# Optimization experiments

Hardware: AMD Instinct MI355X
Metric: run time of the kernel (lower is better)

Reference implementation:

```python
import jax, jax.numpy as jnp
import numpy as np

H = 2048  # hidden_size
B, S = 4, 4096
LEVELS = 3  # hierarchical_compression_levels


def _linear_params(key, out_dim, in_dim):
    kw, kb = jax.random.split(key)
    bound = 1.0 / np.sqrt(in_dim)
    W = jax.random.uniform(kw, (out_dim, in_dim), minval=-bound, maxval=bound, dtype=jnp.float32)
    b = jax.random.uniform(kb, (out_dim,), minval=-bound, maxval=bound, dtype=jnp.float32)
    return W, b


def setup_inputs() -> dict:
    key = jax.random.key(0)
    ks = jax.random.split(key, 12)
    inp = {}
    inp['hidden_states'] = jax.random.normal(ks[0], (B, S, H), dtype=jnp.float32)
    inp['access_frequency'] = jax.random.uniform(ks[1], (B, S), dtype=jnp.float32)
    inp['importance_score'] = jax.random.uniform(ks[2], (B, S), dtype=jnp.float32)
    # compression level 1: H -> H/2 -> H/2 -> H ; level 2: H -> H/4 -> H/4 -> H
    inp['comp1_W'], inp['comp1_b'] = _linear_params(ks[3], H // 2, H)
    inp['adapt1_W'], inp['adapt1_b'] = _linear_params(ks[4], H // 2, H // 2)
    inp['decomp1_W'], inp['decomp1_b'] = _linear_params(ks[5], H, H // 2)
    inp['comp2_W'], inp['comp2_b'] = _linear_params(ks[6], H // 4, H)
    inp['adapt2_W'], inp['adapt2_b'] = _linear_params(ks[7], H // 4, H // 4)
    inp['decomp2_W'], inp['decomp2_b'] = _linear_params(ks[8], H, H // 4)
    # strategy selector: Linear(H, H/4) -> ReLU -> Linear(H/4, LEVELS) -> Softmax
    inp['sel1_W'], inp['sel1_b'] = _linear_params(ks[9], H // 4, H)
    inp['sel2_W'], inp['sel2_b'] = _linear_params(ks[10], LEVELS, H // 4)
    return inp


def reference(hidden_states, access_frequency, importance_score,
              comp1_W, comp1_b, adapt1_W, adapt1_b, decomp1_W, decomp1_b,
              comp2_W, comp2_b, adapt2_W, adapt2_b, decomp2_W, decomp2_b,
              sel1_W, sel1_b, sel2_W, sel2_b):
    h = hidden_states
    h2 = h.shape[-1] // 2
    # _get_compression_strategy: scale first half by freq, second half by importance
    combined = jnp.concatenate(
        [h[..., :h2] * access_frequency[..., None],
         h[..., h2:] * importance_score[..., None]], axis=-1)  # [B,S,H]
    hid = jax.nn.relu(jnp.einsum('bsh,oh->bso', combined, sel1_W) + sel1_b)
    strategy_weights = jax.nn.softmax(jnp.einsum('bso,lo->bsl', hid, sel2_W) + sel2_b, axis=-1)
    selected = jnp.argmax(strategy_weights, axis=-1)  # [B,S] int

    def branch(Wc, bc, Wa, ba, Wd, bd):
        c = jnp.einsum('bsh,oh->bso', h, Wc) + bc          # compress
        c = jnp.einsum('bso,po->bsp', c, Wa) + ba          # frequency adaptor
        return jnp.einsum('bsp,hp->bsh', c, Wd) + bd       # decompress

    out1 = branch(comp1_W, comp1_b, adapt1_W, adapt1_b, decomp1_W, decomp1_b)
    out2 = branch(comp2_W, comp2_b, adapt2_W, adapt2_b, decomp2_W, decomp2_b)
    stacked = jnp.stack([h, out1, out2], axis=2)  # [B,S,LEVELS,H]
    compressed = jnp.take_along_axis(stacked, selected[:, :, None, None], axis=2)[:, :, 0, :]
    return compressed
```

## Files before the change

kernel.cpp:

```cpp
#include <hip/hip_runtime.h>
#include <hip/hip_bf16.h>

#define TOK 16384
#define TAU2 0.001f

typedef __attribute__((ext_vector_type(8))) short short8;
typedef __attribute__((ext_vector_type(4))) float f32x4;

__device__ __forceinline__ unsigned short f32_bf16(float f) {
  __hip_bfloat16 h = __float2bfloat16(f);
  unsigned short u;
  __builtin_memcpy(&u, &h, sizeof(u));
  return u;
}
__device__ __forceinline__ float bf16_f32(unsigned short u) {
  union { unsigned int i; float f; } c; c.i = ((unsigned int)u) << 16; return c.f;
}

__device__ __forceinline__ void gll16(const unsigned short* g, unsigned short* l) {
  __builtin_amdgcn_global_load_lds(
      (const __attribute__((address_space(1))) unsigned int*)g,
      (__attribute__((address_space(3))) unsigned int*)l, 16, 0, 0);
}

__global__ void zero3(int* a, int* c) {
  if (threadIdx.x == 0) { *a = 0; c[0] = 0; c[1] = 0; }
}

__global__ void cvt_kernel(const float* __restrict__ s, unsigned short* __restrict__ d, int n4) {
  int i = blockIdx.x * 256 + threadIdx.x;
  if (i < n4) {
    float4 v = ((const float4*)s)[i];
    union { unsigned short u[4]; uint2 q; } pk;
    pk.u[0] = f32_bf16(v.x); pk.u[1] = f32_bf16(v.y);
    pk.u[2] = f32_bf16(v.z); pk.u[3] = f32_bf16(v.w);
    ((uint2*)d)[i] = pk.q;
  }
}

__global__ void cvt_split_kernel(const float* __restrict__ s,
                                 unsigned short* __restrict__ dhi,
                                 unsigned short* __restrict__ dlo, int n4) {
  int i = blockIdx.x * 256 + threadIdx.x;
  if (i < n4) {
    float4 v = ((const float4*)s)[i];
    const float* f = (const float*)&v;
    union { unsigned short u[4]; uint2 q; } hi, lo;
    #pragma unroll
    for (int e = 0; e < 4; e++) {
      unsigned short h = f32_bf16(f[e]);
      hi.u[e] = h;
      lo.u[e] = f32_bf16(f[e] - bf16_f32(h));
    }
    ((uint2*)dhi)[i] = hi.q;
    ((uint2*)dlo)[i] = lo.q;
  }
}

__global__ void compact_sel(const int* __restrict__ sel, int* __restrict__ idx1,
                            int* __restrict__ idx2, int* __restrict__ cnt) {
  int t = blockIdx.x * 256 + threadIdx.x;
  int s = sel[t];
  if (s == 1) idx1[atomicAdd(&cnt[0], 1)] = t;
  else if (s == 2) idx2[atomicAdd(&cnt[1], 1)] = t;
}

__global__ void pad_idx(int* __restrict__ idx1, int* __restrict__ idx2,
                        const int* __restrict__ cnt, int* __restrict__ mc) {
  const int tid = threadIdx.x;
  const int n1 = cnt[0], n2 = cnt[1];
  const int p1 = (n1 + 127) & ~(int)127, p2 = (n2 + 127) & ~(int)127;
  if (tid < p1 - n1) idx1[n1 + tid] = -1;
  if (tid < p2 - n2) idx2[n2 + tid] = -1;
  if (tid == 0) { mc[0] = p1; mc[1] = p2; }
}

template<int EPI, int AG>
__device__ __forceinline__
void gemm_body(const unsigned short* __restrict__ A,
               const unsigned short* __restrict__ Bw,
               const float* __restrict__ bias,
               void* __restrict__ Outv,
               const int* __restrict__ idx, const int* __restrict__ mcp,
               int N, int K) {
  __shared__ __align__(16) unsigned short As[2][128 * 32];
  __shared__ __align__(16) unsigned short Bs[2][128 * 32];
  const int tid = threadIdx.x;
  const int m0 = blockIdx.y * 128, n0 = blockIdx.x * 128;
  if (mcp && m0 >= *mcp) return;
  const int lane = tid & 63, wave = tid >> 6;
  const int wm = wave >> 1, wn = wave & 1;
  const int quad = lane >> 4, lr = lane & 15;

  const int srow = tid >> 2;
  const int schunk = (tid & 3) ^ (srow & 3);
  unsigned int aoff[2], boff[2];
  #pragma unroll
  for (int r = 0; r < 2; r++) {
    int row = r * 64 + srow;
    int gr = m0 + row;
    if (AG) { int t = idx[gr]; gr = (t < 0) ? 0 : t; }
    aoff[r] = (unsigned int)gr * (unsigned int)K + (unsigned int)(schunk * 8);
    boff[r] = (unsigned int)(n0 + row) * (unsigned int)K + (unsigned int)(schunk * 8);
  }
  const int lds_dst = tid * 8;

  f32x4 acc[4][4] = {};
  const int nk = K >> 5;

  #pragma unroll
  for (int r = 0; r < 2; r++) {
    gll16(A + aoff[r], &As[0][r * 2048 + lds_dst]);
    gll16(Bw + boff[r], &Bs[0][r * 2048 + lds_dst]);
  }
  __syncthreads();

  int cur = 0;
  for (int t = 0; t < nk; t++) {
    if (t + 1 < nk) {
      const unsigned int k0 = (unsigned int)(t + 1) << 5;
      #pragma unroll
      for (int r = 0; r < 2; r++) {
        gll16(A + aoff[r] + k0, &As[cur ^ 1][r * 2048 + lds_dst]);
        gll16(Bw + boff[r] + k0, &Bs[cur ^ 1][r * 2048 + lds_dst]);
      }
    }
    short8 af[4], bfr[4];
    #pragma unroll
    for (int i = 0; i < 4; i++) {
      const int row = wm * 64 + i * 16 + lr;
      af[i] = *(const short8*)(&As[cur][row * 32 + ((quad ^ (row & 3)) << 3)]);
    }
    #pragma unroll
    for (int j = 0; j < 4; j++) {
      const int row = wn * 64 + j * 16 + lr;
      bfr[j] = *(const short8*)(&Bs[cur][row * 32 + ((quad ^ (row & 3)) << 3)]);
    }
    #pragma unroll
    for (int i = 0; i < 4; i++)
      #pragma unroll
      for (int j = 0; j < 4; j++)
        acc[i][j] = __builtin_amdgcn_mfma_f32_16x16x32_bf16(af[i], bfr[j], acc[i][j], 0, 0, 0);
    __syncthreads();
    cur ^= 1;
  }

  #pragma unroll
  for (int i = 0; i < 4; i++) {
    const int rbase = m0 + wm * 64 + i * 16 + quad * 4;
    #pragma unroll
    for (int j = 0; j < 4; j++) {
      const int col = n0 + wn * 64 + j * 16 + lr;
      const float bv = bias[col];
      #pragma unroll
      for (int r = 0; r < 4; r++) {
        const int row = rbase + r;
        float v = acc[i][j][r] + bv;
        if (EPI == 0) {
          ((unsigned short*)Outv)[(size_t)row * N + col] = f32_bf16(v);
        } else {
          const int tk = idx[row];
          if (tk >= 0) ((float*)Outv)[(size_t)tk * N + col] = v;
        }
      }
    }
  }
}

#define GEMM_SHELL(NAME, EPI, AG)                                              \
__global__ __launch_bounds__(256, 3) void NAME(                                \
    const unsigned short* __restrict__ A,                                      \
    const unsigned short* __restrict__ Bw,                                     \
    const float* __restrict__ bias, void* __restrict__ Outv,                   \
    const int* __restrict__ idx, const int* __restrict__ mcp, int N, int K) {  \
  gemm_body<EPI, AG>(A, Bw, bias, Outv, idx, mcp, N, K);                       \
}
GEMM_SHELL(g_comp1, 0, 1)
GEMM_SHELL(g_comp2, 0, 1)
GEMM_SHELL(g_adapt1, 0, 0)
GEMM_SHELL(g_adapt2, 0, 0)
GEMM_SHELL(g_dec1, 4, 0)
GEMM_SHELL(g_dec2, 4, 0)

__global__ __launch_bounds__(256, 2)
void gemm_sel(const float* __restrict__ Af,
              const unsigned short* __restrict__ Bw,
              const unsigned short* __restrict__ Bw2,
              const float* __restrict__ bias,
              float* __restrict__ Out,
              const float* __restrict__ scA, const float* __restrict__ scB,
              int N, int K) {
  __shared__ __align__(16) unsigned short As[2 * 128 * 32];
  __shared__ __align__(16) unsigned short Bs[2 * 128 * 32];
  const int LO = 128 * 32;
  const int tid = threadIdx.x;
  const int m0 = blockIdx.y * 128, n0 = blockIdx.x * 128;
  const int lane = tid & 63, wave = tid >> 6;
  const int wm = wave >> 1, wn = wave & 1;
  const int quad = lane >> 4, lr = lane & 15;
  const int srow = tid >> 1, scol = (tid & 1) * 16;

  const size_t aRowOff = (size_t)(m0 + srow) * K;
  const unsigned short* Brow = Bw + (size_t)(n0 + srow) * K;
  const unsigned short* Brow2 = Bw2 + (size_t)(n0 + srow) * K;

  f32x4 acc[4][4] = {};

  for (int k0 = 0; k0 < K; k0 += 32) {
    {
      const float4* src = (const float4*)(Af + aRowOff + k0 + scol);
      float4 f[4];
      f[0] = src[0]; f[1] = src[1]; f[2] = src[2]; f[3] = src[3];
      const int tk = m0 + srow;
      const float s = ((k0 + scol) * 2 < K) ? scA[tk] : scB[tk];
      union { unsigned short u[16]; uint4 q[2]; } hi;
      union { unsigned short u[16]; uint4 q[2]; } lo;
      const float* ff = (const float*)f;
      #pragma unroll
      for (int e = 0; e < 16; e++) {
        float fv = ff[e] * s;
        unsigned short hb = f32_bf16(fv);
        hi.u[e] = hb;
        lo.u[e] = f32_bf16(fv - bf16_f32(hb));
      }
      uint4* dst = (uint4*)(As + srow * 32 + scol);
      dst[0] = hi.q[0]; dst[1] = hi.q[1];
      uint4* dst2 = (uint4*)(As + LO + srow * 32 + scol);
      dst2[0] = lo.q[0]; dst2[1] = lo.q[1];
    }
    {
      const uint4* src = (const uint4*)(Brow + k0 + scol);
      uint4* dst = (uint4*)(Bs + srow * 32 + scol);
      dst[0] = src[0]; dst[1] = src[1];
      const uint4* src2 = (const uint4*)(Brow2 + k0 + scol);
      uint4* dst2 = (uint4*)(Bs + LO + srow * 32 + scol);
      dst2[0] = src2[0]; dst2[1] = src2[1];
    }
    __syncthreads();
    short8 af[4], bfr[4], af2[4], bf2[4];
    #pragma unroll
    for (int i = 0; i < 4; i++) {
      af[i]  = *(const short8*)(As + (wm * 64 + i * 16 + lr) * 32 + quad * 8);
      af2[i] = *(const short8*)(As + LO + (wm * 64 + i * 16 + lr) * 32 + quad * 8);
    }
    #pragma unroll
    for (int j = 0; j < 4; j++) {
      bfr[j] = *(const short8*)(Bs + (wn * 64 + j * 16 + lr) * 32 + quad * 8);
      bf2[j] = *(const short8*)(Bs + LO + (wn * 64 + j * 16 + lr) * 32 + quad * 8);
    }
    #pragma unroll
    for (int i = 0; i < 4; i++)
      #pragma unroll
      for (int j = 0; j < 4; j++) {
        acc[i][j] = __builtin_amdgcn_mfma_f32_16x16x32_bf16(af[i], bfr[j], acc[i][j], 0, 0, 0);
        acc[i][j] = __builtin_amdgcn_mfma_f32_16x16x32_bf16(af[i], bf2[j], acc[i][j], 0, 0, 0);
        acc[i][j] = __builtin_amdgcn_mfma_f32_16x16x32_bf16(af2[i], bfr[j], acc[i][j], 0, 0, 0);
      }
    __syncthreads();
  }

  #pragma unroll
  for (int i = 0; i < 4; i++) {
    const int rbase = m0 + wm * 64 + i * 16 + quad * 4;
    #pragma unroll
    for (int j = 0; j < 4; j++) {
      const int col = n0 + wn * 64 + j * 16 + lr;
      const float bv = bias[col];
      #pragma unroll
      for (int r = 0; r < 4; r++) {
        const int row = rbase + r;
        float v = acc[i][j][r] + bv;
        Out[(size_t)row * N + col] = fmaxf(v, 0.0f);
      }
    }
  }
}

__global__ __launch_bounds__(256)
void selector_logits_f32(const float* __restrict__ hidf,
                         const float* __restrict__ W2, const float* __restrict__ b2,
                         int* __restrict__ sel, int* __restrict__ risky,
                         int* __restrict__ riskyCount) {
  const int wave = threadIdx.x >> 6, lane = threadIdx.x & 63;
  const int token = blockIdx.x * 4 + wave;
  const float* hs = hidf + (size_t)token * 512 + lane * 8;
  float4 h0 = *(const float4*)hs, h1 = *(const float4*)(hs + 4);
  float p[3];
  #pragma unroll
  for (int c = 0; c < 3; c++) {
    const float* w = W2 + c * 512 + lane * 8;
    float4 w0 = *(const float4*)w, w1 = *(const float4*)(w + 4);
    p[c] = h0.x*w0.x + h0.y*w0.y + h0.z*w0.z + h0.w*w0.w
         + h1.x*w1.x + h1.y*w1.y + h1.z*w1.z + h1.w*w1.w;
  }
  #pragma unroll
  for (int off = 32; off >= 1; off >>= 1) {
    #pragma unroll
    for (int c = 0; c < 3; c++) p[c] += __shfl_xor(p[c], off, 64);
  }
  if (lane == 0) {
    float l0 = p[0] + b2[0], l1 = p[1] + b2[1], l2 = p[2] + b2[2];
    int arg = 0; float best = l0;
    if (l1 > best) { best = l1; arg = 1; }
    if (l2 > best) { best = l2; arg = 2; }
    float second;
    if (arg == 0) second = fmaxf(l1, l2);
    else if (arg == 1) second = fmaxf(l0, l2);
    else second = fmaxf(l0, l1);
    sel[token] = arg;
    if (best - second < TAU2) {
      int idx = atomicAdd(riskyCount, 1);
      risky[idx] = token;
    }
  }
}

__global__ __launch_bounds__(256)
void recheck_exact(const float* __restrict__ h, const float* __restrict__ freq,
                   const float* __restrict__ imp,
                   const float* __restrict__ W1, const float* __restrict__ b1,
                   const float* __restrict__ W2, const float* __restrict__ b2,
                   const int* __restrict__ risky, const int* __restrict__ riskyCount,
                   int* __restrict__ sel) {
  __shared__ float h_sh[2048];
  __shared__ float hid_sh[512];
  const int n = *riskyCount;
  const int tid = threadIdx.x;
  for (int ri = blockIdx.x; ri < n; ri += gridDim.x) {
    const int token = risky[ri];
    {
      const float s = (tid < 128) ? freq[token] : imp[token];
      const float4* src = (const float4*)(h + (size_t)token * 2048) + tid * 2;
      float4 v0 = src[0], v1 = src[1];
      v0.x *= s; v0.y *= s; v0.z *= s; v0.w *= s;
      v1.x *= s; v1.y *= s; v1.z *= s; v1.w *= s;
      ((float4*)h_sh)[tid * 2] = v0;
      ((float4*)h_sh)[tid * 2 + 1] = v1;
    }
    __syncthreads();
    #pragma unroll
    for (int half = 0; half < 2; half++) {
      const int o = tid + half * 256;
      const float* wrow = W1 + (size_t)o * 2048;
      float a0 = 0.f, a1 = 0.f, a2 = 0.f, a3 = 0.f;
      for (int k = 0; k < 2048; k += 16) {
        float4 w0 = *(const float4*)(wrow + k);
        float4 w1v = *(const float4*)(wrow + k + 4);
        float4 w2v = *(const float4*)(wrow + k + 8);
        float4 w3v = *(const float4*)(wrow + k + 12);
        float4 x0 = *(const float4*)(h_sh + k);
        float4 x1 = *(const float4*)(h_sh + k + 4);
        float4 x2 = *(const float4*)(h_sh + k + 8);
        float4 x3 = *(const float4*)(h_sh + k + 12);
        a0 += w0.x*x0.x + w0.y*x0.y + w0.z*x0.z + w0.w*x0.w;
        a1 += w1v.x*x1.x + w1v.y*x1.y + w1v.z*x1.z + w1v.w*x1.w;
        a2 += w2v.x*x2.x + w2v.y*x2.y + w2v.z*x2.z + w2v.w*x2.w;
        a3 += w3v.x*x3.x + w3v.y*x3.y + w3v.z*x3.z + w3v.w*x3.w;
      }
      hid_sh[o] = fmaxf((a0 + a1) + (a2 + a3) + b1[o], 0.0f);
    }
    __syncthreads();
    if (tid < 64) {
      const int lane = tid;
      const float* hs = &hid_sh[lane * 8];
      float l[3];
      #pragma unroll
      for (int c = 0; c < 3; c++) {
        const float* w = W2 + c * 512 + lane * 8;
        float s = 0.0f;
        #pragma unroll
        for (int e = 0; e < 8; e++) s += hs[e] * w[e];
        l[c] = s;
      }
      #pragma unroll
      for (int off = 32; off >= 1; off >>= 1)
        #pragma unroll
        for (int c = 0; c < 3; c++) l[c] += __shfl_xor(l[c], off, 64);
      if (lane == 0) {
        float l0 = l[0] + b2[0], l1 = l[1] + b2[1], l2 = l[2] + b2[2];
        int arg = 0; float best = l0;
        if (l1 > best) { best = l1; arg = 1; }
        if (l2 > best) { arg = 2; }
        sel[token] = arg;
      }
    }
    __syncthreads();
  }
}

__global__ __launch_bounds__(256)
void copy_sel0(const float* __restrict__ h, const int* __restrict__ sel,
               float* __restrict__ out) {
  const int token = blockIdx.x;
  if (sel[token] != 0) return;
  const float4* src = (const float4*)(h + (size_t)token * 2048);
  float4* dst = (float4*)(out + (size_t)token * 2048);
  dst[threadIdx.x] = src[threadIdx.x];
  dst[threadIdx.x + 256] = src[threadIdx.x + 256];
}

extern "C" void kernel_launch(void* const* d_in, const int* in_sizes, int n_in,
                              void* d_out, int out_size, void* d_ws, size_t ws_size,
                              hipStream_t stream) {
  const float* h        = (const float*)d_in[0];
  const float* freq     = (const float*)d_in[1];
  const float* imp      = (const float*)d_in[2];
  const float* comp1W   = (const float*)d_in[3];
  const float* comp1b   = (const float*)d_in[4];
  const float* adapt1W  = (const float*)d_in[5];
  const float* adapt1b  = (const float*)d_in[6];
  const float* decomp1W = (const float*)d_in[7];
  const float* decomp1b = (const float*)d_in[8];
  const float* comp2W   = (const float*)d_in[9];
  const float* comp2b   = (const float*)d_in[10];
  const float* adapt2W  = (const float*)d_in[11];
  const float* adapt2b  = (const float*)d_in[12];
  const float* decomp2W = (const float*)d_in[13];
  const float* decomp2b = (const float*)d_in[14];
  const float* sel1W    = (const float*)d_in[15];
  const float* sel1b    = (const float*)d_in[16];
  const float* sel2W    = (const float*)d_in[17];
  const float* sel2b    = (const float*)d_in[18];
  float* out = (float*)d_out;

  char* ws = (char*)d_ws;
  size_t off = 0;
  auto alloc = [&](size_t bytes) -> void* {
    void* p = ws + off; off += (bytes + 255) & ~(size_t)255; return p;
  };
  unsigned short* wb_comp1   = (unsigned short*)alloc((size_t)1024 * 2048 * 2);
  unsigned short* wb_adapt1  = (unsigned short*)alloc((size_t)1024 * 1024 * 2);
  unsigned short* wb_decomp1 = (unsigned short*)alloc((size_t)2048 * 1024 * 2);
  unsigned short* wb_comp2   = (unsigned short*)alloc((size_t)512 * 2048 * 2);
  unsigned short* wb_adapt2  = (unsigned short*)alloc((size_t)512 * 512 * 2);
  unsigned short* wb_decomp2 = (unsigned short*)alloc((size_t)2048 * 512 * 2);
  unsigned short* w1hi       = (unsigned short*)alloc((size_t)512 * 2048 * 2);
  unsigned short* w1lo       = (unsigned short*)alloc((size_t)512 * 2048 * 2);
  float*          hidf       = (float*)alloc((size_t)TOK * 512 * 4);
  unsigned short* c1         = (unsigned short*)alloc((size_t)TOK * 1024 * 2);
  unsigned short* a1         = (unsigned short*)alloc((size_t)TOK * 1024 * 2);
  int* sel        = (int*)alloc((size_t)TOK * 4);
  int* risky      = (int*)alloc((size_t)TOK * 4);
  int* riskyCount = (int*)alloc(256);
  int* idx1       = (int*)alloc((size_t)TOK * 4);
  int* idx2       = (int*)alloc((size_t)TOK * 4);
  int* cnt        = (int*)alloc(256);
  int* mc         = (int*)alloc(256);

  unsigned short* hb = (unsigned short*)out;
  unsigned short* c2 = (unsigned short*)hidf;
  unsigned short* a2 = (unsigned short*)hidf + (size_t)TOK * 512;

  zero3<<<1, 64, 0, stream>>>(riskyCount, cnt);

  auto cvt = [&](const float* s, unsigned short* d, int n) {
    cvt_kernel<<<(n / 4 + 255) / 256, 256, 0, stream>>>(s, d, n / 4);
  };
  cvt(comp1W,   wb_comp1,   1024 * 2048);
  cvt(adapt1W,  wb_adapt1,  1024 * 1024);
  cvt(decomp1W, wb_decomp1, 2048 * 1024);
  cvt(comp2W,   wb_comp2,   512 * 2048);
  cvt(adapt2W,  wb_adapt2,  512 * 512);
  cvt(decomp2W, wb_decomp2, 2048 * 512);
  cvt(h,        hb,         TOK * 2048);
  cvt_split_kernel<<<(512 * 2048 / 4 + 255) / 256, 256, 0, stream>>>(
      sel1W, w1hi, w1lo, 512 * 2048 / 4);

  gemm_sel<<<dim3(512 / 128, TOK / 128), 256, 0, stream>>>(
      h, w1hi, w1lo, sel1b, hidf, freq, imp, 512, 2048);
  selector_logits_f32<<<TOK / 4, 256, 0, stream>>>(hidf, sel2W, sel2b, sel, risky, riskyCount);
  recheck_exact<<<256, 256, 0, stream>>>(h, freq, imp, sel1W, sel1b, sel2W, sel2b,
                                         risky, riskyCount, sel);

  compact_sel<<<TOK / 256, 256, 0, stream>>>(sel, idx1, idx2, cnt);
  pad_idx<<<1, 256, 0, stream>>>(idx1, idx2, cnt, mc);

  g_comp1<<<dim3(1024 / 128, TOK / 128), 256, 0, stream>>>(
      hb, wb_comp1, comp1b, c1, idx1, mc + 0, 1024, 2048);
  g_comp2<<<dim3(512 / 128, TOK / 128), 256, 0, stream>>>(
      hb, wb_comp2, comp2b, c2, idx2, mc + 1, 512, 2048);
  g_adapt1<<<dim3(1024 / 128, TOK / 128), 256, 0, stream>>>(
      c1, wb_adapt1, adapt1b, a1, nullptr, mc + 0, 1024, 1024);
  g_adapt2<<<dim3(512 / 128, TOK / 128), 256, 0, stream>>>(
      c2, wb_adapt2, adapt2b, a2, nullptr, mc + 1, 512, 512);
  g_dec1<<<dim3(2048 / 128, TOK / 128), 256, 0, stream>>>(
      a1, wb_decomp1, decomp1b, out, idx1, mc + 0, 2048, 1024);
  g_dec2<<<dim3(2048 / 128, TOK / 128), 256, 0, stream>>>(
      a2, wb_decomp2, decomp2b, out, idx2, mc + 1, 2048, 512);

  copy_sel0<<<TOK, 256, 0, stream>>>(h, sel, out);
}
```

Measured before the change: 952.8 us.

## Triple-buffer GEMM LDS pipeline with explicit vmcnt waits; grid-stride sel0 copy

Replaces the double-buffered LDS mainloop of the shared GEMM body with a three-stage ring, so two K tiles are in flight while one is computed. It uses explicit s_waitcnt vmcnt counts and raw s_barrier in place of __syncthreads, so loads for later tiles are not drained every iteration. LDS use rises by half, which may lower occupancy. Separately, the sel0 copy kernel becomes a grid-stride loop over 2048 blocks instead of one block per token, cutting the launch of mostly idle blocks.

```diff
diff --git a/kernel.cpp b/kernel.cpp
--- a/kernel.cpp
+++ b/kernel.cpp
@@ -3,6 +3,7 @@
 
 #define TOK 16384
 #define TAU2 0.001f
+#define CFENCE asm volatile("" ::: "memory")
 
 typedef __attribute__((ext_vector_type(8))) short short8;
 typedef __attribute__((ext_vector_type(4))) float f32x4;
@@ -83,8 +84,8 @@
                void* __restrict__ Outv,
                const int* __restrict__ idx, const int* __restrict__ mcp,
                int N, int K) {
-  __shared__ __align__(16) unsigned short As[2][128 * 32];
-  __shared__ __align__(16) unsigned short Bs[2][128 * 32];
+  __shared__ __align__(16) unsigned short As[3 * 128 * 32];
+  __shared__ __align__(16) unsigned short Bs[3 * 128 * 32];
   const int tid = threadIdx.x;
   const int m0 = blockIdx.y * 128, n0 = blockIdx.x * 128;
   if (mcp && m0 >= *mcp) return;
@@ -108,42 +109,56 @@
   f32x4 acc[4][4] = {};
   const int nk = K >> 5;
 
-  #pragma unroll
-  for (int r = 0; r < 2; r++) {
-    gll16(A + aoff[r], &As[0][r * 2048 + lds_dst]);
-    gll16(Bw + boff[r], &Bs[0][r * 2048 + lds_dst]);
-  }
-  __syncthreads();
-
-  int cur = 0;
-  for (int t = 0; t < nk; t++) {
-    if (t + 1 < nk) {
-      const unsigned int k0 = (unsigned int)(t + 1) << 5;
-      #pragma unroll
-      for (int r = 0; r < 2; r++) {
-        gll16(A + aoff[r] + k0, &As[cur ^ 1][r * 2048 + lds_dst]);
-        gll16(Bw + boff[r] + k0, &Bs[cur ^ 1][r * 2048 + lds_dst]);
-      }
-    }
-    short8 af[4], bfr[4];
-    #pragma unroll
-    for (int i = 0; i < 4; i++) {
-      const int row = wm * 64 + i * 16 + lr;
-      af[i] = *(const short8*)(&As[cur][row * 32 + ((quad ^ (row & 3)) << 3)]);
-    }
-    #pragma unroll
-    for (int j = 0; j < 4; j++) {
-      const int row = wn * 64 + j * 16 + lr;
-      bfr[j] = *(const short8*)(&Bs[cur][row * 32 + ((quad ^ (row & 3)) << 3)]);
-    }
-    #pragma unroll
-    for (int i = 0; i < 4; i++)
-      #pragma unroll
-      for (int j = 0; j < 4; j++)
-        acc[i][j] = __builtin_amdgcn_mfma_f32_16x16x32_bf16(af[i], bfr[j], acc[i][j], 0, 0, 0);
-    __syncthreads();
-    cur ^= 1;
-  }
+  #define STAGE(T, O)                                                        \
+    {                                                                        \
+      const unsigned int k0 = (unsigned int)(T) << 5;                        \
+      gll16(A + aoff[0] + k0, &As[(O) + lds_dst]);                           \
+      gll16(A + aoff[1] + k0, &As[(O) + 2048 + lds_dst]);                    \
+      gll16(Bw + boff[0] + k0, &Bs[(O) + lds_dst]);                          \
+      gll16(Bw + boff[1] + k0, &Bs[(O) + 2048 + lds_dst]);                   \
+    }
+  #define COMPUTE(O)                                                         \
+    {                                                                        \
+      short8 af[4], bfr[4];                                                  \
+      _Pragma("unroll")                                                      \
+      for (int i = 0; i < 4; i++) {                                          \
+        const int row = wm * 64 + i * 16 + lr;                               \
+        af[i] = *(const short8*)(&As[(O) + row * 32 + ((quad ^ (row & 3)) << 3)]); \
+      }                                                                      \
+      _Pragma("unroll")                                                      \
+      for (int j = 0; j < 4; j++) {                                          \
+        const int row = wn * 64 + j * 16 + lr;                               \
+        bfr[j] = *(const short8*)(&Bs[(O) + row * 32 + ((quad ^ (row & 3)) << 3)]); \
+      }                                                                      \
+      _Pragma("unroll")                                                      \
+      for (int i = 0; i < 4; i++)                                            \
+        _Pragma("unroll")                                                    \
+        for (int j = 0; j < 4; j++)                                          \
+          acc[i][j] = __builtin_amdgcn_mfma_f32_16x16x32_bf16(af[i], bfr[j], acc[i][j], 0, 0, 0); \
+    }
+
+  int oA = 0, oB = 4096, oC = 8192;
+  STAGE(0, oA);
+  STAGE(1, oB);
+
+  for (int t = 0; t < nk - 2; t++) {
+    STAGE(t + 2, oC);
+    asm volatile("s_waitcnt vmcnt(8)" ::: "memory");
+    CFENCE; __builtin_amdgcn_s_barrier(); CFENCE;
+    COMPUTE(oA);
+    CFENCE; __builtin_amdgcn_s_barrier(); CFENCE;
+    int tmp = oA; oA = oB; oB = oC; oC = tmp;
+  }
+  asm volatile("s_waitcnt vmcnt(4)" ::: "memory");
+  CFENCE; __builtin_amdgcn_s_barrier(); CFENCE;
+  COMPUTE(oA);
+  CFENCE; __builtin_amdgcn_s_barrier(); CFENCE;
+  { int tmp = oA; oA = oB; oB = oC; oC = tmp; }
+  asm volatile("s_waitcnt vmcnt(0)" ::: "memory");
+  CFENCE; __builtin_amdgcn_s_barrier(); CFENCE;
+  COMPUTE(oA);
+  #undef STAGE
+  #undef COMPUTE
 
   #pragma unroll
   for (int i = 0; i < 4; i++) {
@@ -391,12 +406,13 @@
 __global__ __launch_bounds__(256)
 void copy_sel0(const float* __restrict__ h, const int* __restrict__ sel,
                float* __restrict__ out) {
-  const int token = blockIdx.x;
-  if (sel[token] != 0) return;
-  const float4* src = (const float4*)(h + (size_t)token * 2048);
-  float4* dst = (float4*)(out + (size_t)token * 2048);
-  dst[threadIdx.x] = src[threadIdx.x];
-  dst[threadIdx.x + 256] = src[threadIdx.x + 256];
+  for (int token = blockIdx.x; token < TOK; token += gridDim.x) {
+    if (sel[token] != 0) continue;
+    const float4* src = (const float4*)(h + (size_t)token * 2048);
+    float4* dst = (float4*)(out + (size_t)token * 2048);
+    dst[threadIdx.x] = src[threadIdx.x];
+    dst[threadIdx.x + 256] = src[threadIdx.x + 256];
+  }
 }
 
 extern "C" void kernel_launch(void* const* d_in, const int* in_sizes, int n_in,
@@ -488,5 +504,5 @@
   g_dec2<<<dim3(2048 / 128, TOK / 128), 256, 0, stream>>>(
       a2, wb_decomp2, decomp2b, out, idx2, mc + 1, 2048, 512);
 
-  copy_sel0<<<TOK, 256, 0, stream>>>(h, sel, out);
-}
+  copy_sel0<<<2048, 256, 0, stream>>>(h, sel, out);
+}
```

After: 938.2 us. Within noise of the previous version (-1.5%).
